# Kernel optimization log

Hardware: AMD Instinct MI355X
Metric: run time of the kernel (lower is better)

The kernel has to match this reference:

```python
import jax, jax.numpy as jnp
import numpy as np

DIM = 768; HEADS = 12; DIM_HEAD = 64; INNER = HEADS * DIM_HEAD
GT_HEADS = 8; GT_DH = 64; GT_INNER = GT_HEADS * GT_DH
W = 128; DEPTH = 4; NUM_TOKENS = 32000; SEQ = 4096; MAX_SEQ = 4096; B = 1
FF_MULT = 4


def layer_norm(x, g, b, eps=1e-5):
    mu = x.mean(-1, keepdims=True)
    var = ((x - mu) ** 2).mean(-1, keepdims=True)
    return (x - mu) / jnp.sqrt(var + eps) * g + b


def ffn(x, w1_, b1_, w2_, b2_):
    return jax.nn.gelu(x @ w1_ + b1_, approximate=False) @ w2_ + b2_


def global_attn(g, wqkv, wo_, bo_):
    # full causal MHA over the (few) global tokens
    b, n, _ = g.shape
    q, k, v = jnp.split(g @ wqkv, 3, axis=-1)
    sh = lambda t: t.reshape(b, n, GT_HEADS, GT_DH).transpose(0, 2, 1, 3)  # b h n d
    q, k, v = sh(q), sh(k), sh(v)
    sim = jnp.einsum('bhid,bhjd->bhij', q, k) * (GT_DH ** -0.5)
    cm = jnp.triu(jnp.ones((n, n), dtype=bool), k=1)
    sim = jnp.where(cm, -jnp.finfo(sim.dtype).max, sim)
    attn = jax.nn.softmax(sim, axis=-1)
    out = jnp.einsum('bhij,bhjd->bhid', attn, v)
    out = out.transpose(0, 2, 1, 3).reshape(b, n, GT_INNER)
    return out @ wo_ + bo_


def local_attn(x, g, wq_, wkv_, wo_, bo_):
    # windowed look-back attention + global-token keys. n assumed multiple of W.
    b, n, _ = x.shape
    bh = b * HEADS
    buckets = n // W
    sh = lambda t, m: t.reshape(b, m, HEADS, DIM_HEAD).transpose(0, 2, 1, 3).reshape(bh, m, DIM_HEAD)
    q = sh(x @ wq_, n)
    k, v = jnp.split(x @ wkv_, 2, axis=-1)
    k, v = sh(k, n), sh(v, n)
    win = lambda t: t.reshape(bh, buckets, W, DIM_HEAD)
    q, k, v = win(q), win(k), win(v)
    kp = jnp.pad(k, ((0, 0), (1, 0), (0, 0), (0, 0)))
    # NOTE: faithfully replicates upstream bug -- the lambda in the torch code
    # builds BOTH k and v from k, so v becomes the k look-back concat too.
    k2 = jnp.concatenate([kp[:, :-1], kp[:, 1:]], axis=2)  # [bh, buckets, 2W, d]
    v2 = k2
    local_j = 2 * W
    # global tokens (last one dropped)
    gt = g[:, :-1]
    ng = gt.shape[1]
    gk, gv = jnp.split(gt @ wkv_, 2, axis=-1)
    gsh = lambda t: t.reshape(b, ng, HEADS, DIM_HEAD).transpose(0, 2, 1, 3).reshape(bh, ng, DIM_HEAD)
    gk = jnp.broadcast_to(gsh(gk)[:, None], (bh, buckets, ng, DIM_HEAD))
    gv = jnp.broadcast_to(gsh(gv)[:, None], (bh, buckets, ng, DIM_HEAD))
    kf = jnp.concatenate([gk, k2], axis=2)
    vf = jnp.concatenate([gv, v2], axis=2)
    sim = jnp.einsum('bwid,bwjd->bwij', q, kf) * (DIM_HEAD ** -0.5)
    mv = -jnp.finfo(sim.dtype).max
    m_local = jnp.triu(jnp.ones((W, local_j), dtype=bool), k=local_j - W + 1)
    m_local = jnp.broadcast_to(m_local[None], (buckets, W, local_j))
    m_glob = jnp.triu(jnp.ones((buckets, ng), dtype=bool), k=ng - W)
    m_glob = jnp.broadcast_to(m_glob[:, None, :], (buckets, W, ng))
    cmask = jnp.concatenate([m_glob, m_local], axis=-1)[None]
    sim = jnp.where(cmask, mv, sim)
    attn = jax.nn.softmax(sim, axis=-1)
    out = jnp.einsum('bwij,bwjd->bwid', attn, vf)
    out = out.reshape(b, HEADS, n, DIM_HEAD).transpose(0, 2, 1, 3).reshape(b, n, INNER)
    return out @ wo_ + bo_


def setup_inputs() -> dict:
    ks = iter(jax.random.split(jax.random.key(0), 64))
    nrm = lambda shape: jax.random.normal(next(ks), shape, jnp.float32) * 0.02
    return {
        'x': jax.random.randint(next(ks), (B, SEQ), 0, NUM_TOKENS),
        'token_emb': nrm((NUM_TOKENS, DIM)),
        'pos_emb': nrm((MAX_SEQ, DIM)),
        'global_pos_emb': nrm((MAX_SEQ // W, DIM)),
        'gt_ln1_g': jnp.ones((DIM,)), 'gt_ln1_b': jnp.zeros((DIM,)),
        'gt_wqkv': nrm((DIM, 3 * GT_INNER)), 'gt_wo': nrm((GT_INNER, DIM)), 'gt_bo': jnp.zeros((DIM,)),
        'gt_ln2_g': jnp.ones((DIM,)), 'gt_ln2_b': jnp.zeros((DIM,)),
        'gt_w1': nrm((DIM, FF_MULT * DIM)), 'gt_b1': jnp.zeros((FF_MULT * DIM,)),
        'gt_w2': nrm((FF_MULT * DIM, DIM)), 'gt_b2': jnp.zeros((DIM,)),
        'ln1_g': jnp.ones((DEPTH, DIM)), 'ln1_b': jnp.zeros((DEPTH, DIM)),
        'wq': nrm((DEPTH, DIM, INNER)), 'wkv': nrm((DEPTH, DIM, 2 * INNER)),
        'wo': nrm((DEPTH, INNER, DIM)), 'bo': jnp.zeros((DEPTH, DIM)),
        'ln2_g': jnp.ones((DEPTH, DIM)), 'ln2_b': jnp.zeros((DEPTH, DIM)),
        'w1': nrm((DEPTH, DIM, FF_MULT * DIM)), 'b1': jnp.zeros((DEPTH, FF_MULT * DIM)),
        'w2': nrm((DEPTH, FF_MULT * DIM, DIM)), 'b2': jnp.zeros((DEPTH, DIM)),
        'f_ln_g': jnp.ones((DIM,)), 'f_ln_b': jnp.zeros((DIM,)),
        'w_logits': nrm((DIM, NUM_TOKENS)), 'b_logits': jnp.zeros((NUM_TOKENS,)),
    }


def reference(x, token_emb, pos_emb, global_pos_emb,
              gt_ln1_g, gt_ln1_b, gt_wqkv, gt_wo, gt_bo,
              gt_ln2_g, gt_ln2_b, gt_w1, gt_b1, gt_w2, gt_b2,
              ln1_g, ln1_b, wq, wkv, wo, bo,
              ln2_g, ln2_b, w1, b1, w2, b2,
              f_ln_g, f_ln_b, w_logits, b_logits):
    b, n = x.shape
    buckets = n // W  # n % W == 0 for chosen shapes -> r = 0 branch
    h = token_emb[x]                                    # [b, n, dim]
    g = h.reshape(b, buckets, W, DIM).mean(axis=2)      # pooled global tokens
    h = h + pos_emb[:n][None]
    g = g + global_pos_emb[:buckets][None]
    for l in range(DEPTH):
        g = g + global_attn(layer_norm(g, gt_ln1_g, gt_ln1_b), gt_wqkv, gt_wo, gt_bo)
        g = g + ffn(layer_norm(g, gt_ln2_g, gt_ln2_b), gt_w1, gt_b1, gt_w2, gt_b2)
        h = h + local_attn(layer_norm(h, ln1_g[l], ln1_b[l]), g, wq[l], wkv[l], wo[l], bo[l])
        h = h + ffn(layer_norm(h, ln2_g[l], ln2_b[l]), w1[l], b1[l], w2[l], b2[l])
    return layer_norm(h, f_ln_g, f_ln_b) @ w_logits + b_logits
```

## Files before the change

kernel.cpp:

```cpp
#include <hip/hip_runtime.h>
#include <hip/hip_bf16.h>


#define DIMM   768
#define SEQLEN 4096
#define NHEADS 12
#define DH     64
#define WWIN   128
#define NBUCK  32
#define NDEPTH 4
#define FFDIM  3072
#define NTOK   32000
#define QKLD   1536
#define NEG_MAX (-3.402823466e38f)

typedef unsigned short u16;
typedef __attribute__((ext_vector_type(8))) short bf16x8;
typedef __attribute__((ext_vector_type(4))) float f32x4;

#define GLOAD16(gp, lp) \
  __builtin_amdgcn_global_load_lds((const __attribute__((address_space(1))) void*)(gp), \
                                   (__attribute__((address_space(3))) void*)(lp), 16, 0, 0)

#define BAR()      __builtin_amdgcn_s_barrier()
#define SBAR()     __builtin_amdgcn_sched_barrier(0)
#define PRIO(x)    __builtin_amdgcn_s_setprio(x)
#define VMDRAIN()  asm volatile("s_waitcnt vmcnt(0)" ::: "memory")

__global__ __launch_bounds__(256) void embed_kernel(
    const int* __restrict__ x, const float* __restrict__ tok,
    const float* __restrict__ pos, float* __restrict__ h) {
  int row = blockIdx.x;
  int t = threadIdx.x;
  int tk = x[row];
  const float* te = tok + (size_t)tk * DIMM;
  const float* pe = pos + (size_t)row * DIMM;
  float* hr = h + (size_t)row * DIMM;
  hr[t]       = te[t]       + pe[t];
  hr[t + 256] = te[t + 256] + pe[t + 256];
  hr[t + 512] = te[t + 512] + pe[t + 512];
}

__global__ __launch_bounds__(256) void ln_kernel(
    const float* __restrict__ in, const float* __restrict__ gam,
    const float* __restrict__ bet, __hip_bfloat16* __restrict__ out) {
  int row = blockIdx.x;
  int t = threadIdx.x;
  const float* xr = in + (size_t)row * DIMM;
  float v0 = xr[t], v1 = xr[t + 256], v2 = xr[t + 512];
  float s  = v0 + v1 + v2;
  float s2 = v0 * v0 + v1 * v1 + v2 * v2;
  #pragma unroll
  for (int o = 32; o > 0; o >>= 1) {
    s  += __shfl_down(s, o);
    s2 += __shfl_down(s2, o);
  }
  __shared__ float red[2][4];
  int wid = t >> 6, lane = t & 63;
  if (lane == 0) { red[0][wid] = s; red[1][wid] = s2; }
  __syncthreads();
  if (t == 0) {
    float ts  = red[0][0] + red[0][1] + red[0][2] + red[0][3];
    float ts2 = red[1][0] + red[1][1] + red[1][2] + red[1][3];
    float mean = ts * (1.0f / DIMM);
    float var  = ts2 * (1.0f / DIMM) - mean * mean;
    red[0][0] = mean;
    red[1][0] = rsqrtf(var + 1e-5f);
  }
  __syncthreads();
  float mean = red[0][0], rstd = red[1][0];
  __hip_bfloat16* orow = out + (size_t)row * DIMM;
  orow[t]       = __float2bfloat16((v0 - mean) * rstd * gam[t]       + bet[t]);
  orow[t + 256] = __float2bfloat16((v1 - mean) * rstd * gam[t + 256] + bet[t + 256]);
  orow[t + 512] = __float2bfloat16((v2 - mean) * rstd * gam[t + 512] + bet[t + 512]);
}

__global__ __launch_bounds__(256) void wprep_kernel(
    const float* __restrict__ src, u16* __restrict__ dst,
    int ldsrc, int Krows, size_t sls, size_t dls) {
  __shared__ float tile[32][33];
  int l = blockIdx.z;
  int n0 = blockIdx.x * 32, k0 = blockIdx.y * 32;
  int tx = threadIdx.x & 31, ty = threadIdx.x >> 5;
  const float* s = src + (size_t)l * sls;
  u16* d = dst + (size_t)l * dls;
  #pragma unroll
  for (int i = 0; i < 4; ++i)
    tile[ty + i * 8][tx] = s[(size_t)(k0 + ty + i * 8) * ldsrc + n0 + tx];
  __syncthreads();
  #pragma unroll
  for (int i = 0; i < 4; ++i) {
    __hip_bfloat16 b = __float2bfloat16(tile[tx][ty + i * 8]);
    d[(size_t)(n0 + ty + i * 8) * Krows + k0 + tx] = *(u16*)&b;
  }
}

template<int TBM, int TBN>
__global__ __launch_bounds__(256) void gemm_bf16(
    const u16* __restrict__ A, const u16* __restrict__ Bt,
    const float* __restrict__ bias, const float* __restrict__ resid,
    void* __restrict__ Cv, int K, int ldc, int act, int cbf16) {
  constexpr int MFR = TBM / 32;
  constexpr int NFR = TBN / 32;
  constexpr int G = (TBM == 128 ? 2 : 1) + (TBN == 128 ? 2 : 1);
  __shared__ u16 As[2][TBM * 32];
  __shared__ u16 Bs[2][TBN * 32];
  int tid = threadIdx.x;
  int wave = tid >> 6, lane = tid & 63;

  int lin = blockIdx.y * gridDim.x + blockIdx.x;
  int cpx = (gridDim.x * gridDim.y) >> 3;
  int swz = (lin & 7) * cpx + (lin >> 3);
  int by = swz % gridDim.y;
  int bx = swz / gridDim.y;

  int bm = by * TBM, bn = bx * TBN;
  int wm = (wave >> 1) * (TBM / 2), wn = (wave & 1) * (TBN / 2);
  int fr = lane & 15, fq = lane >> 4;

  f32x4 acc[MFR][NFR];
  #pragma unroll
  for (int i = 0; i < MFR; ++i)
    #pragma unroll
    for (int j = 0; j < NFR; ++j) acc[i][j] = (f32x4){0.f, 0.f, 0.f, 0.f};

  int r0 = tid >> 2;
  int kb = ((tid & 3) ^ ((r0 >> 1) & 3)) * 8;
  const u16* aptr = A + (size_t)(bm + r0) * K + kb;
  const u16* bptr = Bt + (size_t)(bn + r0) * K + kb;
  int sA = (fq ^ ((fr >> 1) & 3)) * 8;

#define STAGE_TILE(buf) do {                                          \
    char* lA = (char*)(&As[buf][0]) + wave * 1024;                    \
    char* lB = (char*)(&Bs[buf][0]) + wave * 1024;                    \
    GLOAD16(aptr, lA);                                                \
    if constexpr (TBM == 128) GLOAD16(aptr + (size_t)64 * K, lA + 4096); \
    GLOAD16(bptr, lB);                                                \
    if constexpr (TBN == 128) GLOAD16(bptr + (size_t)64 * K, lB + 4096); \
    aptr += 32; bptr += 32;                                           \
  } while (0)

  const int nk = K >> 5;
  STAGE_TILE(0);
  STAGE_TILE(1);

  for (int t = 0; t < nk; ++t) {
    const int cur = t & 1;
    if (t + 1 < nk) {
      if constexpr (G == 2) asm volatile("s_waitcnt vmcnt(2)" ::: "memory");
      else if constexpr (G == 3) asm volatile("s_waitcnt vmcnt(3)" ::: "memory");
      else asm volatile("s_waitcnt vmcnt(4)" ::: "memory");
    } else {
      VMDRAIN();
    }
    BAR();
    bf16x8 af[MFR], bfr[NFR];
    #pragma unroll
    for (int m = 0; m < MFR; ++m)
      af[m] = *(const bf16x8*)&As[cur][(wm + m * 16 + fr) * 32 + sA];
    #pragma unroll
    for (int n = 0; n < NFR; ++n)
      bfr[n] = *(const bf16x8*)&Bs[cur][(wn + n * 16 + fr) * 32 + sA];
    asm volatile("s_waitcnt lgkmcnt(0)" ::: "memory");
    SBAR();
    BAR();
    if (t + 2 < nk) STAGE_TILE(cur);
    PRIO(1);
    #pragma unroll
    for (int m = 0; m < MFR; ++m)
      #pragma unroll
      for (int n = 0; n < NFR; ++n)
        acc[m][n] = __builtin_amdgcn_mfma_f32_16x16x32_bf16(af[m], bfr[n], acc[m][n], 0, 0, 0);
    PRIO(0);
  }
#undef STAGE_TILE

  #pragma unroll
  for (int m = 0; m < MFR; ++m) {
    #pragma unroll
    for (int rr = 0; rr < 4; ++rr) {
      int row = bm + wm + m * 16 + fq * 4 + rr;
      #pragma unroll
      for (int n = 0; n < NFR; ++n) {
        int col = bn + wn + n * 16 + fr;
        float v = acc[m][n][rr];
        if (bias) v += bias[col];
        if (act) v = 0.5f * v * (1.0f + erff(v * 0.70710678118654752f));
        if (resid) v += resid[(size_t)row * ldc + col];
        if (cbf16) {
          __hip_bfloat16 b = __float2bfloat16(v);
          ((u16*)Cv)[(size_t)row * ldc + col] = *(u16*)&b;
        } else {
          ((float*)Cv)[(size_t)row * ldc + col] = v;
        }
      }
    }
  }
}

__global__ __launch_bounds__(512, 1) void gemm256(
    const u16* __restrict__ A, const u16* __restrict__ Bt,
    const float* __restrict__ bias, float* __restrict__ C, int K, int ldc) {
  __shared__ __align__(16) char GL[131072];
  const int tid = threadIdx.x;
  const int wave = tid >> 6, lane = tid & 63;
  const int fr = lane & 15, fq = lane >> 4;

  int lin = blockIdx.y * gridDim.x + blockIdx.x;
  int cpx = (gridDim.x * gridDim.y) >> 3;
  int swz = (lin & 7) * cpx + (lin >> 3);
  int by = swz % gridDim.y;
  int bx = swz / gridDim.y;

  const int bm = by * 256, bn = bx * 256;
  const int wm = (wave >> 2) * 128, wn = (wave & 3) * 64;

  const int r_in = tid >> 3;
  const int g_log = (tid & 7) ^ (r_in & 7);
  const size_t a_base = (size_t)(bm + r_in) * K + g_log * 8;
  const size_t b_base = (size_t)(bn + r_in) * K + g_log * 8;
  const int lds_st = wave * 1024;

  const int slot0 = ((fq) ^ (fr & 7)) * 16;
  const int slot1 = ((4 + fq) ^ (fr & 7)) * 16;

  f32x4 acc[8][4];
  #pragma unroll
  for (int i = 0; i < 8; ++i)
    #pragma unroll
    for (int j = 0; j < 4; ++j) acc[i][j] = (f32x4){0.f, 0.f, 0.f, 0.f};

  bf16x8 aq[4][2], bp0[2][2], bp1[2][2];

#define STG4(gb, ldsoff) do {                                   \
    const u16* g_ = (gb);                                       \
    GLOAD16(g_,                  GL + (ldsoff) + lds_st);       \
    GLOAD16(g_ + (size_t)64 * K,  GL + (ldsoff) + 8192 + lds_st);  \
    GLOAD16(g_ + (size_t)128 * K, GL + (ldsoff) + 16384 + lds_st); \
    GLOAD16(g_ + (size_t)192 * K, GL + (ldsoff) + 24576 + lds_st); \
  } while (0)

#define RD_AQ(QOFF, c)                                                   \
    _Pragma("unroll") for (int mm = 0; mm < 4; ++mm) {                   \
      const char* p_ = GL + (c) * 32768 + (wm + (QOFF) + mm * 16 + fr) * 128; \
      aq[mm][0] = *(const bf16x8*)(p_ + slot0);                          \
      aq[mm][1] = *(const bf16x8*)(p_ + slot1);                          \
    }
#define RD_BP(BP, NOFF, c)                                               \
    _Pragma("unroll") for (int nn = 0; nn < 2; ++nn) {                   \
      const char* p_ = GL + 65536 + (c) * 32768 + (wn + (NOFF) + nn * 16 + fr) * 128; \
      BP[nn][0] = *(const bf16x8*)(p_ + slot0);                          \
      BP[nn][1] = *(const bf16x8*)(p_ + slot1);                          \
    }
#define MMA8(MB, NB, BP)                                                 \
    _Pragma("unroll") for (int mm = 0; mm < 4; ++mm)                     \
      _Pragma("unroll") for (int nn = 0; nn < 2; ++nn)                   \
        _Pragma("unroll") for (int kk = 0; kk < 2; ++kk)                 \
          acc[(MB) + mm][(NB) + nn] = __builtin_amdgcn_mfma_f32_16x16x32_bf16( \
              aq[mm][kk], BP[nn][kk], acc[(MB) + mm][(NB) + nn], 0, 0, 0);

  const int nk = K >> 6;
  STG4(A + a_base, 0);
  STG4(Bt + b_base, 65536);
  VMDRAIN();
  BAR();

  for (int t = 0; t < nk; ++t) {
    const int c = t & 1;
    if (t + 1 < nk) STG4(A + a_base + (size_t)(t + 1) * 64, (c ^ 1) * 32768);
    RD_AQ(0, c); RD_BP(bp0, 0, c);
    BAR();
    PRIO(1); MMA8(0, 0, bp0); PRIO(0);
    SBAR(); BAR();
    if (t + 1 < nk) STG4(Bt + b_base + (size_t)(t + 1) * 64, 65536 + (c ^ 1) * 32768);
    RD_BP(bp1, 32, c);
    BAR();
    PRIO(1); MMA8(0, 2, bp1); PRIO(0);
    SBAR(); BAR();
    RD_AQ(64, c);
    BAR();
    PRIO(1); MMA8(4, 2, bp1); PRIO(0);
    SBAR(); BAR();
    PRIO(1); MMA8(4, 0, bp0); PRIO(0);
    SBAR();
    VMDRAIN();
    BAR();
  }
#undef STG4
#undef RD_AQ
#undef RD_BP
#undef MMA8

  #pragma unroll
  for (int m = 0; m < 8; ++m) {
    #pragma unroll
    for (int rr = 0; rr < 4; ++rr) {
      int row = bm + wm + m * 16 + fq * 4 + rr;
      #pragma unroll
      for (int n = 0; n < 4; ++n) {
        int col = bn + wn + n * 16 + fr;
        C[(size_t)row * ldc + col] = acc[m][n][rr] + bias[col];
      }
    }
  }
}

__global__ __launch_bounds__(256, 1) void attn_mfma(
    const u16* __restrict__ QK, u16* __restrict__ CTX) {
  __shared__ __align__(16) char LDS[131072];
  char* Kl = LDS;
  char* Kt = LDS + 32768;
  const int w = blockIdx.x, hd = blockIdx.y;
  const int tid = threadIdx.x;
  const int wave = tid >> 6, lane = tid & 63;
  const int fr = lane & 15, fq = lane >> 4;
  char* Pw = LDS + 65536 + wave * 16384;

  {
    const int j = tid;
    const int p = (w - 1) * WWIN + j;
    bf16x8 kv[8];
    if (p >= 0) {
      const bf16x8* src = (const bf16x8*)(QK + (size_t)p * QKLD + DIMM + hd * DH);
      #pragma unroll
      for (int g = 0; g < 8; ++g) kv[g] = src[g];
    } else {
      #pragma unroll
      for (int g = 0; g < 8; ++g) kv[g] = (bf16x8){0, 0, 0, 0, 0, 0, 0, 0};
    }
    #pragma unroll
    for (int g = 0; g < 8; ++g)
      *(bf16x8*)(Kl + j * 128 + ((g ^ (j & 7)) * 16)) = kv[g];
    #pragma unroll
    for (int g = 0; g < 8; ++g)
      #pragma unroll
      for (int e = 0; e < 8; ++e) {
        const int d = g * 8 + e;
        *(u16*)(Kt + d * 512 + (((j >> 3) ^ (d & 7)) * 16) + ((j & 7) * 2)) =
            (u16)kv[g][e];
      }
  }

  bf16x8 aq[2][2];
  #pragma unroll
  for (int m = 0; m < 2; ++m)
    #pragma unroll
    for (int kk = 0; kk < 2; ++kk)
      aq[m][kk] = *(const bf16x8*)(QK +
          (size_t)(w * WWIN + wave * 32 + m * 16 + fr) * QKLD + hd * DH + kk * 32 + fq * 8);

  __syncthreads();

  f32x4 sacc[2][16];
  #pragma unroll
  for (int m = 0; m < 2; ++m)
    #pragma unroll
    for (int n = 0; n < 16; ++n) sacc[m][n] = (f32x4){0.f, 0.f, 0.f, 0.f};
  #pragma unroll
  for (int n = 0; n < 16; ++n) {
    #pragma unroll
    for (int kk = 0; kk < 2; ++kk) {
      bf16x8 bk = *(const bf16x8*)(Kl + (n * 16 + fr) * 128 +
                                   (((kk * 4 + fq) ^ (fr & 7)) * 16));
      #pragma unroll
      for (int m = 0; m < 2; ++m)
        sacc[m][n] = __builtin_amdgcn_mfma_f32_16x16x32_bf16(aq[m][kk], bk, sacc[m][n], 0, 0, 0);
    }
  }

  float inv_[2][4];
  #pragma unroll
  for (int m = 0; m < 2; ++m) {
    #pragma unroll
    for (int rr = 0; rr < 4; ++rr) {
      const int r = wave * 32 + m * 16 + fq * 4 + rr;
      float pv[16];
      float mx = NEG_MAX;
      #pragma unroll
      for (int n = 0; n < 16; ++n) {
        const int j = n * 16 + fr;
        float s = sacc[m][n][rr] * 0.125f;
        bool vis = (j <= r + 128);
        pv[n] = vis ? s : NEG_MAX;
        if (vis) mx = fmaxf(mx, s);
      }
      #pragma unroll
      for (int o = 1; o < 16; o <<= 1) mx = fmaxf(mx, __shfl_xor(mx, o));
      float sum = 0.f;
      #pragma unroll
      for (int n = 0; n < 16; ++n) {
        float p = (pv[n] != NEG_MAX) ? __expf(pv[n] - mx) : 0.f;
        pv[n] = p;
        sum += p;
      }
      #pragma unroll
      for (int o = 1; o < 16; o <<= 1) sum += __shfl_xor(sum, o);
      inv_[m][rr] = 1.0f / sum;
      const int rl = m * 16 + fq * 4 + rr;
      #pragma unroll
      for (int n = 0; n < 16; ++n) {
        __hip_bfloat16 b = __float2bfloat16(pv[n]);
        const int gj = n * 2 + (fr >> 3);
        *(u16*)(Pw + rl * 512 + ((gj ^ (rl & 7)) * 16) + ((fr & 7) * 2)) = *(u16*)&b;
      }
    }
  }
  __syncthreads();

  f32x4 oacc[2][4];
  #pragma unroll
  for (int m = 0; m < 2; ++m)
    #pragma unroll
    for (int nd = 0; nd < 4; ++nd) oacc[m][nd] = (f32x4){0.f, 0.f, 0.f, 0.f};
  #pragma unroll
  for (int kc = 0; kc < 8; ++kc) {
    const int slot = ((kc * 4 + fq) ^ (fr & 7)) * 16;
    bf16x8 pa[2];
    #pragma unroll
    for (int m = 0; m < 2; ++m)
      pa[m] = *(const bf16x8*)(Pw + (m * 16 + fr) * 512 + slot);
    #pragma unroll
    for (int nd = 0; nd < 4; ++nd) {
      bf16x8 kb = *(const bf16x8*)(Kt + (nd * 16 + fr) * 512 + slot);
      #pragma unroll
      for (int m = 0; m < 2; ++m)
        oacc[m][nd] = __builtin_amdgcn_mfma_f32_16x16x32_bf16(pa[m], kb, oacc[m][nd], 0, 0, 0);
    }
  }

  #pragma unroll
  for (int m = 0; m < 2; ++m)
    #pragma unroll
    for (int nd = 0; nd < 4; ++nd)
      #pragma unroll
      for (int rr = 0; rr < 4; ++rr) {
        const int row = w * WWIN + wave * 32 + m * 16 + fq * 4 + rr;
        const int col = hd * DH + nd * 16 + fr;
        __hip_bfloat16 b = __float2bfloat16(oacc[m][nd][rr] * inv_[m][rr]);
        CTX[(size_t)row * DIMM + col] = *(u16*)&b;
      }
}

extern "C" void kernel_launch(void* const* d_in, const int* in_sizes, int n_in,
                              void* d_out, int out_size, void* d_ws, size_t ws_size,
                              hipStream_t stream) {
  const int*   x         = (const int*)d_in[0];
  const float* token_emb = (const float*)d_in[1];
  const float* pos_emb   = (const float*)d_in[2];
  const float* ln1_g = (const float*)d_in[15];
  const float* ln1_b = (const float*)d_in[16];
  const float* wq    = (const float*)d_in[17];
  const float* wkv   = (const float*)d_in[18];
  const float* wo    = (const float*)d_in[19];
  const float* bo    = (const float*)d_in[20];
  const float* ln2_g = (const float*)d_in[21];
  const float* ln2_b = (const float*)d_in[22];
  const float* w1    = (const float*)d_in[23];
  const float* b1    = (const float*)d_in[24];
  const float* w2    = (const float*)d_in[25];
  const float* b2    = (const float*)d_in[26];
  const float* f_ln_g = (const float*)d_in[27];
  const float* f_ln_b = (const float*)d_in[28];
  const float* w_logits = (const float*)d_in[29];
  const float* b_logits = (const float*)d_in[30];
  float* out = (float*)d_out;

  char* ob = (char*)d_out;
  float* h    = (float*)(ob + 0);
  u16* qk     = (u16*)(ob + 12582912);
  u16* ctx    = (u16*)(ob + 25165824);
  u16* mid    = (u16*)(ob + 31457280);
  u16* warena = (u16*)(ob + 56623104);
  const size_t WQ_SZ = (size_t)DIMM * DIMM;
  const size_t W1_SZ = (size_t)DIMM * FFDIM;
  const size_t LW = 3 * WQ_SZ + 2 * W1_SZ;
  u16* qkw_t = warena;
  u16* wo_t  = warena + 2 * WQ_SZ;
  u16* w1_t  = warena + 3 * WQ_SZ;
  u16* w2_t  = warena + 3 * WQ_SZ + W1_SZ;

  u16* wlog_t = (u16*)d_ws;
  __hip_bfloat16* lnbuf = (__hip_bfloat16*)((char*)d_ws + 49152000);

  wprep_kernel<<<dim3(24, 24, 4), 256, 0, stream>>>(wq,  qkw_t,         DIMM,   DIMM,  WQ_SZ,   LW);
  wprep_kernel<<<dim3(24, 24, 4), 256, 0, stream>>>(wkv, qkw_t + WQ_SZ, 2*DIMM, DIMM,  2*WQ_SZ, LW);
  wprep_kernel<<<dim3(24, 24, 4), 256, 0, stream>>>(wo,  wo_t,          DIMM,   DIMM,  WQ_SZ,   LW);
  wprep_kernel<<<dim3(96, 24, 4), 256, 0, stream>>>(w1,  w1_t,          FFDIM,  DIMM,  W1_SZ,   LW);
  wprep_kernel<<<dim3(24, 96, 4), 256, 0, stream>>>(w2,  w2_t,          DIMM,   FFDIM, W1_SZ,   LW);
  wprep_kernel<<<dim3(1000, 24, 1), 256, 0, stream>>>(w_logits, wlog_t, NTOK, DIMM, 0, 0);

  embed_kernel<<<SEQLEN, 256, 0, stream>>>(x, token_emb, pos_emb, h);

  for (int l = 0; l < NDEPTH; ++l) {
    ln_kernel<<<SEQLEN, 256, 0, stream>>>(h, ln1_g + l * DIMM, ln1_b + l * DIMM, lnbuf);
    gemm_bf16<64, 128><<<dim3(12, 64), 256, 0, stream>>>(
        (const u16*)lnbuf, qkw_t + l * LW, nullptr, nullptr, qk, DIMM, QKLD, 0, 1);
    attn_mfma<<<dim3(NBUCK, NHEADS), 256, 0, stream>>>(qk, ctx);
    gemm_bf16<64, 64><<<dim3(12, 64), 256, 0, stream>>>(
        ctx, wo_t + l * LW, bo + l * DIMM, h, h, DIMM, DIMM, 0, 0);
    ln_kernel<<<SEQLEN, 256, 0, stream>>>(h, ln2_g + l * DIMM, ln2_b + l * DIMM, lnbuf);
    gemm_bf16<64, 128><<<dim3(24, 64), 256, 0, stream>>>(
        (const u16*)lnbuf, w1_t + l * LW, b1 + l * FFDIM, nullptr, mid, DIMM, FFDIM, 1, 1);
    gemm_bf16<64, 64><<<dim3(12, 64), 256, 0, stream>>>(
        mid, w2_t + l * LW, b2 + l * DIMM, h, h, FFDIM, DIMM, 0, 0);
  }

  ln_kernel<<<SEQLEN, 256, 0, stream>>>(h, f_ln_g, f_ln_b, lnbuf);
  gemm256<<<dim3(NTOK / 256, SEQLEN / 256), 512, 0, stream>>>(
      (const u16*)lnbuf, wlog_t, b_logits, out, DIMM, NTOK);
}
```

Baseline: 1.145 ms.

## Restructure gemm256 main loop into 4-stage K=32 pipeline with 3 loads in flight

Replaces the double-buffered K=64 mainloop of the 256x256 GEMM with a four-buffer ring of K=32 slices, keeping three stages of global-to-LDS loads in flight and using vmcnt-based waits instead of full drains. The LDS swizzle changes to a 4-chunk XOR pattern for 64-byte rows, and each iteration runs one barrier, one fragment read and 32 MFMAs. This is meant to hide global memory latency better and cut the number of barriers per K step. In exchange the K slices are smaller per barrier, and correctness now depends on exact vmcnt counts.

```diff
diff --git a/kernel.cpp b/kernel.cpp
--- a/kernel.cpp
+++ b/kernel.cpp
@@ -215,14 +215,13 @@
   const int bm = by * 256, bn = bx * 256;
   const int wm = (wave >> 2) * 128, wn = (wave & 3) * 64;
 
-  const int r_in = tid >> 3;
-  const int g_log = (tid & 7) ^ (r_in & 7);
-  const size_t a_base = (size_t)(bm + r_in) * K + g_log * 8;
-  const size_t b_base = (size_t)(bn + r_in) * K + g_log * 8;
+  const int r_in = tid >> 2;
+  const int g_swz = (tid & 3) ^ ((r_in >> 1) & 3);
+  const size_t a_base = (size_t)(bm + r_in) * K + g_swz * 8;
+  const size_t b_base = (size_t)(bn + r_in) * K + g_swz * 8;
   const int lds_st = wave * 1024;
 
-  const int slot0 = ((fq) ^ (fr & 7)) * 16;
-  const int slot1 = ((4 + fq) ^ (fr & 7)) * 16;
+  const int sA = (fq ^ ((fr >> 1) & 3)) * 16;
 
   f32x4 acc[8][4];
   #pragma unroll
@@ -230,66 +229,47 @@
     #pragma unroll
     for (int j = 0; j < 4; ++j) acc[i][j] = (f32x4){0.f, 0.f, 0.f, 0.f};
 
-  bf16x8 aq[4][2], bp0[2][2], bp1[2][2];
-
-#define STG4(gb, ldsoff) do {                                   \
-    const u16* g_ = (gb);                                       \
-    GLOAD16(g_,                  GL + (ldsoff) + lds_st);       \
-    GLOAD16(g_ + (size_t)64 * K,  GL + (ldsoff) + 8192 + lds_st);  \
-    GLOAD16(g_ + (size_t)128 * K, GL + (ldsoff) + 16384 + lds_st); \
-    GLOAD16(g_ + (size_t)192 * K, GL + (ldsoff) + 24576 + lds_st); \
+#define STG(s, b) do {                                                  \
+    const u16* ga = A + a_base + (size_t)(s) * 32;                      \
+    const u16* gb = Bt + b_base + (size_t)(s) * 32;                     \
+    GLOAD16(ga,                   GL + (b) * 16384 + lds_st);           \
+    GLOAD16(ga + (size_t)128 * K, GL + (b) * 16384 + 8192 + lds_st);    \
+    GLOAD16(gb,                   GL + 65536 + (b) * 16384 + lds_st);   \
+    GLOAD16(gb + (size_t)128 * K, GL + 65536 + (b) * 16384 + 8192 + lds_st); \
   } while (0)
 
-#define RD_AQ(QOFF, c)                                                   \
-    _Pragma("unroll") for (int mm = 0; mm < 4; ++mm) {                   \
-      const char* p_ = GL + (c) * 32768 + (wm + (QOFF) + mm * 16 + fr) * 128; \
-      aq[mm][0] = *(const bf16x8*)(p_ + slot0);                          \
-      aq[mm][1] = *(const bf16x8*)(p_ + slot1);                          \
-    }
-#define RD_BP(BP, NOFF, c)                                               \
-    _Pragma("unroll") for (int nn = 0; nn < 2; ++nn) {                   \
-      const char* p_ = GL + 65536 + (c) * 32768 + (wn + (NOFF) + nn * 16 + fr) * 128; \
-      BP[nn][0] = *(const bf16x8*)(p_ + slot0);                          \
-      BP[nn][1] = *(const bf16x8*)(p_ + slot1);                          \
-    }
-#define MMA8(MB, NB, BP)                                                 \
-    _Pragma("unroll") for (int mm = 0; mm < 4; ++mm)                     \
-      _Pragma("unroll") for (int nn = 0; nn < 2; ++nn)                   \
-        _Pragma("unroll") for (int kk = 0; kk < 2; ++kk)                 \
-          acc[(MB) + mm][(NB) + nn] = __builtin_amdgcn_mfma_f32_16x16x32_bf16( \
-              aq[mm][kk], BP[nn][kk], acc[(MB) + mm][(NB) + nn], 0, 0, 0);
-
-  const int nk = K >> 6;
-  STG4(A + a_base, 0);
-  STG4(Bt + b_base, 65536);
-  VMDRAIN();
-  BAR();
+  const int nk = K >> 5;
+  STG(0, 0);
+  STG(1, 1);
+  STG(2, 2);
 
   for (int t = 0; t < nk; ++t) {
-    const int c = t & 1;
-    if (t + 1 < nk) STG4(A + a_base + (size_t)(t + 1) * 64, (c ^ 1) * 32768);
-    RD_AQ(0, c); RD_BP(bp0, 0, c);
+    const int buf = t & 3;
+    if (t <= nk - 3)      asm volatile("s_waitcnt vmcnt(8)" ::: "memory");
+    else if (t == nk - 2) asm volatile("s_waitcnt vmcnt(4)" ::: "memory");
+    else                  VMDRAIN();
     BAR();
-    PRIO(1); MMA8(0, 0, bp0); PRIO(0);
-    SBAR(); BAR();
-    if (t + 1 < nk) STG4(Bt + b_base + (size_t)(t + 1) * 64, 65536 + (c ^ 1) * 32768);
-    RD_BP(bp1, 32, c);
-    BAR();
-    PRIO(1); MMA8(0, 2, bp1); PRIO(0);
-    SBAR(); BAR();
-    RD_AQ(64, c);
-    BAR();
-    PRIO(1); MMA8(4, 2, bp1); PRIO(0);
-    SBAR(); BAR();
-    PRIO(1); MMA8(4, 0, bp0); PRIO(0);
+    if (t + 3 < nk) STG(t + 3, (t + 3) & 3);
+    bf16x8 aq[8], bq[4];
+    const char* pa = GL + buf * 16384;
+    const char* pb = GL + 65536 + buf * 16384;
+    #pragma unroll
+    for (int m = 0; m < 8; ++m)
+      aq[m] = *(const bf16x8*)(pa + (wm + m * 16 + fr) * 64 + sA);
+    #pragma unroll
+    for (int n = 0; n < 4; ++n)
+      bq[n] = *(const bf16x8*)(pb + (wn + n * 16 + fr) * 64 + sA);
+    asm volatile("s_waitcnt lgkmcnt(0)" ::: "memory");
     SBAR();
-    VMDRAIN();
-    BAR();
-  }
-#undef STG4
-#undef RD_AQ
-#undef RD_BP
-#undef MMA8
+    PRIO(1);
+    #pragma unroll
+    for (int m = 0; m < 8; ++m)
+      #pragma unroll
+      for (int n = 0; n < 4; ++n)
+        acc[m][n] = __builtin_amdgcn_mfma_f32_16x16x32_bf16(aq[m], bq[n], acc[m][n], 0, 0, 0);
+    PRIO(0);
+  }
+#undef STG
 
   #pragma unroll
   for (int m = 0; m < 8; ++m) {
```

Result: no change. 1.155 ms (+0.8%).
